# Kernel optimization log

Hardware: AMD Instinct MI355X
Metric: run time of the kernel (lower is better)

Reference implementation:

```python
import jax, jax.numpy as jnp
import numpy as np
import math

B, S, E, H = 4, 2048, 1024, 16
D = E // H  # head_dim = 64


def setup_inputs() -> dict:
    key = jax.random.key(0)
    ks = jax.random.split(key, 12)
    sc = 1.0 / math.sqrt(E)
    inp = {
        "x": jax.random.normal(ks[0], (B, S, E), jnp.float32),
        "mask": jnp.ones((B, S), jnp.int32),
        "text_array": jax.random.normal(ks[1], (B, E), jnp.float32),
        # attention projections, torch Linear convention W:[out,in]
        "Wq": jax.random.normal(ks[2], (E, E), jnp.float32) * sc,
        "bq": jnp.zeros((E,), jnp.float32),
        "Wk": jax.random.normal(ks[3], (E, E), jnp.float32) * sc,
        "bk": jnp.zeros((E,), jnp.float32),
        "Wv": jax.random.normal(ks[4], (E, E), jnp.float32) * sc,
        "bv": jnp.zeros((E,), jnp.float32),
        "Wo": jax.random.normal(ks[5], (E, E), jnp.float32) * sc,
        "bo": jnp.zeros((E,), jnp.float32),
        # TwoLayerMLP head: E -> E//2 -> 1
        "W1": jax.random.normal(ks[6], (E // 2, E), jnp.float32) * sc,
        "b1": jnp.zeros((E // 2,), jnp.float32),
        "W2": jax.random.normal(ks[7], (1, E // 2), jnp.float32) * (1.0 / math.sqrt(E // 2)),
        "b2": jnp.zeros((1,), jnp.float32),
    }
    return inp


def reference(x, mask, text_array, Wq, bq, Wk, bk, Wv, bv, Wo, bo, W1, b1, W2, b2):
    b, s, e = x.shape
    # projections -> [B, S, H, D]
    Q = (x @ Wq.T + bq).reshape(b, s, H, D)
    K = (x @ Wk.T + bk).reshape(b, s, H, D)
    V = (x @ Wv.T + bv).reshape(b, s, H, D)
    # scores [B, H, Sq, Sk]
    scores = jnp.einsum("bqhd,bkhd->bhqk", Q, K) / jnp.sqrt(jnp.asarray(D, x.dtype))
    neg_inf = jnp.asarray(-jnp.inf, scores.dtype)
    scores = jnp.where(mask[:, None, None, :] == 0, neg_inf, scores)
    attn = jax.nn.softmax(scores, axis=-1)  # dropout is identity in eval
    out = jnp.einsum("bhqk,bkhd->bqhd", attn, V).reshape(b, s, e)
    out = out @ Wo.T + bo  # out_proj (out_dropout identity)
    out = out.mean(axis=1)  # [B, E]
    out = out / jnp.linalg.norm(out, axis=-1, keepdims=True)
    out = out - text_array
    h = jax.nn.relu(out @ W1.T + b1)
    score = jnp.tanh(h @ W2.T + b2)  # [B, 1]
    return score
```

## Files before the change

### kernel.cpp

```cpp
#include <hip/hip_runtime.h>

typedef unsigned short ushort_t;
typedef unsigned int uint32;
typedef __attribute__((ext_vector_type(8))) short short8;
typedef __attribute__((ext_vector_type(4))) float f32x4;
typedef __attribute__((ext_vector_type(2))) uint32 uint32x2;

__device__ __forceinline__ ushort_t f2bf(float f) {
  uint32 u = __builtin_bit_cast(uint32, f);
  u = (u + 0x7fffu + ((u >> 16) & 1u)) >> 16;
  return (ushort_t)u;
}

__device__ __forceinline__ float fast_exp2(float x) {
#if __has_builtin(__builtin_amdgcn_exp2f)
  return __builtin_amdgcn_exp2f(x);
#else
  return exp2f(x);
#endif
}

__device__ __forceinline__ uint32 cvt_pk_bf16(float lo, float hi) {
  uint32 r;
  asm("v_cvt_pk_bf16_f32 %0, %1, %2" : "=v"(r) : "v"(lo), "v"(hi));
  return r;
}

__device__ __forceinline__ void gload_lds16(const void* g, void* l) {
  __builtin_amdgcn_global_load_lds(
      (const __attribute__((address_space(1))) void*)g,
      (__attribute__((address_space(3))) void*)l, 16, 0, 0);
}

#define MFMA16(a, b, c) __builtin_amdgcn_mfma_f32_16x16x32_bf16((a), (b), (c), 0, 0, 0)

__global__ void cvt_kernel(const float* __restrict__ src, ushort_t* __restrict__ dst, int n8) {
  int i = blockIdx.x * 256 + threadIdx.x;
  if (i >= n8) return;
  const f32x4* s4 = (const f32x4*)src;
  f32x4 a = s4[2 * i], b = s4[2 * i + 1];
  short8 o;
  o[0] = (short)f2bf(a.x); o[1] = (short)f2bf(a.y); o[2] = (short)f2bf(a.z); o[3] = (short)f2bf(a.w);
  o[4] = (short)f2bf(b.x); o[5] = (short)f2bf(b.y); o[6] = (short)f2bf(b.z); o[7] = (short)f2bf(b.w);
  *(short8*)(dst + 8 * i) = o;
}

__global__ void maskbias_kernel(const int* __restrict__ mask, float* __restrict__ bias, int n) {
  int i = blockIdx.x * 256 + threadIdx.x;
  if (i < n) bias[i] = mask[i] ? 0.f : -30000.f;
}

template <int MODE>
__global__ __launch_bounds__(256, 2) void gemm_bt(const ushort_t* __restrict__ A,
                                                  const ushort_t* __restrict__ Bt,
                                                  const float* __restrict__ bias,
                                                  ushort_t* __restrict__ C, int M, int N, int K,
                                                  float scale) {
  __shared__ ushort_t As[2][128 * 32];
  __shared__ ushort_t Bs[2][128 * 32];
  const int tid = threadIdx.x;
  const int w = tid >> 6, l = tid & 63;
  const int wr = w >> 1, wc = w & 1;
  const int lr = l & 15, g = l >> 4;
  const int bm = blockIdx.y * 128, bn = blockIdx.x * 128;

  const char* gA = (const char*)(A + (size_t)(bm + w * 32 + (l >> 2)) * K + (l & 3) * 8);
  const char* gB = (const char*)(Bt + (size_t)(bn + w * 32 + (l >> 2)) * K + (l & 3) * 8);
  const size_t rowstep = (size_t)16 * K * 2;

  f32x4 acc[4][4] = {};

  auto stage = [&](int buf, int k0) {
    char* dA = (char*)&As[buf][0] + w * 2048;
    char* dB = (char*)&Bs[buf][0] + w * 2048;
    const char* sA = gA + (size_t)k0 * 2;
    const char* sB = gB + (size_t)k0 * 2;
    gload_lds16(sA, dA);
    gload_lds16(sA + rowstep, dA + 1024);
    gload_lds16(sB, dB);
    gload_lds16(sB + rowstep, dB + 1024);
  };

  stage(0, 0);
  __syncthreads();

  const int nk = K >> 5;
  for (int kk = 0; kk < nk; kk++) {
    const int cur = kk & 1;
    if (kk + 1 < nk) stage(cur ^ 1, (kk + 1) << 5);
    short8 af[4], bf[4];
#pragma unroll
    for (int fm = 0; fm < 4; fm++)
      af[fm] = *(const short8*)(&As[cur][(wr * 64 + fm * 16 + lr) * 32 + g * 8]);
#pragma unroll
    for (int fn = 0; fn < 4; fn++)
      bf[fn] = *(const short8*)(&Bs[cur][(wc * 64 + fn * 16 + lr) * 32 + g * 8]);
#pragma unroll
    for (int fm = 0; fm < 4; fm++)
#pragma unroll
      for (int fn = 0; fn < 4; fn++) acc[fm][fn] = MFMA16(af[fm], bf[fn], acc[fm][fn]);
    __syncthreads();
  }

  if (MODE == 0) {
#pragma unroll
    for (int fn = 0; fn < 4; fn++) {
      int col = bn + wc * 64 + fn * 16 + lr;
      float bv = bias[col];
      int h = col >> 6, d = col & 63;
#pragma unroll
      for (int fm = 0; fm < 4; fm++) {
        int rowb = bm + wr * 64 + fm * 16 + g * 4;
#pragma unroll
        for (int j = 0; j < 4; j++) {
          int row = rowb + j;
          int b = row >> 11, s = row & 2047;
          float v = (acc[fm][fn][j] + bv) * scale;
          C[((size_t)(b * 16 + h) * 2048 + s) * 64 + d] = f2bf(v);
        }
      }
    }
  } else {
#pragma unroll
    for (int fm = 0; fm < 4; fm++) {
#pragma unroll
      for (int j = 0; j < 4; j++) {
        int row = bm + wr * 64 + fm * 16 + g * 4 + j;
        float bv = bias[row];
#pragma unroll
        for (int fn = 0; fn < 4; fn++) {
          int col = bn + wc * 64 + fn * 16 + lr;
          C[(size_t)row * N + col] = f2bf(acc[fm][fn][j] + bv);
        }
      }
    }
  }
}

__global__ __launch_bounds__(256, 2) void attn_kernel(const ushort_t* __restrict__ Qb,
                                                      const ushort_t* __restrict__ Kb,
                                                      const ushort_t* __restrict__ Vt,
                                                      const float* __restrict__ mbias,
                                                      float* __restrict__ meanO) {
  __shared__ ushort_t Ks[2][64 * 64];
  __shared__ ushort_t Vs[2][64 * 64];
  __shared__ ushort_t Ps[4][16 * 64];
  __shared__ float bias[2048];

  const int tid = threadIdx.x;
  const int w = tid >> 6, l = tid & 63;
  const int g = l >> 4, qi = l & 15;
  const int xr = qi & 7;
  const int qblk = blockIdx.x, bh = blockIdx.y;
  const int b = bh >> 4, h = bh & 15;
  const int q0 = qblk * 128 + w * 32;

  short8 qf[2][2];
#pragma unroll
  for (int qh = 0; qh < 2; qh++) {
    const ushort_t* qp = Qb + ((size_t)bh * 2048 + q0 + qh * 16 + qi) * 64 + g * 8;
    qf[qh][0] = *(const short8*)qp;
    qf[qh][1] = *(const short8*)(qp + 32);
  }

  {
    const f32x4* bsrc = (const f32x4*)(mbias + b * 2048);
    f32x4* bdst = (f32x4*)bias;
    bdst[tid] = bsrc[tid];
    bdst[tid + 256] = bsrc[tid + 256];
  }

  const int srow = l >> 3;
  const int sch = (l & 7) ^ srow;
  const char* gK = (const char*)Kb + ((size_t)bh * 2048 + w * 8 + srow) * 128 + sch * 16;
  const char* gV = (const char*)Vt +
                   (((size_t)(h * 64 + w * 8 + srow)) * 8192 + (size_t)b * 2048) * 2 + sch * 16;

  auto stage = [&](int buf, int t) {
    const char* sK = gK + (size_t)t * (64 * 128);
    const char* sV = gV + (size_t)t * 128;
    char* dK = (char*)&Ks[buf][0] + w * 1024;
    char* dV = (char*)&Vs[buf][0] + w * 1024;
    gload_lds16(sK, dK);
    gload_lds16(sK + 32 * 128, dK + 4096);
    gload_lds16(sV, dV);
    gload_lds16(sV + (size_t)32 * 16384, dV + 4096);
  };

  float mrun[2] = {-1e30f, -1e30f}, lsum[2] = {0.f, 0.f};
  f32x4 ot[2][4] = {};

  stage(0, 0);
  __syncthreads();

  for (int t = 0; t < 32; t++) {
    const int cur = t & 1;
    if (t < 31) stage(cur ^ 1, t + 1);

    short8 kf[4][2];
#pragma unroll
    for (int fn = 0; fn < 4; fn++) {
      const ushort_t* kr = &Ks[cur][(fn * 16 + qi) * 64];
      kf[fn][0] = *(const short8*)(kr + (g ^ xr) * 8);
      kf[fn][1] = *(const short8*)(kr + ((4 + g) ^ xr) * 8);
    }
    short8 vf[2][4];
#pragma unroll
    for (int tt = 0; tt < 2; tt++)
#pragma unroll
      for (int fd = 0; fd < 4; fd++)
        vf[tt][fd] = *(const short8*)(&Vs[cur][(fd * 16 + qi) * 64] + ((tt * 4 + g) ^ xr) * 8);
    f32x4 bvec[4];
#pragma unroll
    for (int fn = 0; fn < 4; fn++) bvec[fn] = *(const f32x4*)&bias[t * 64 + fn * 16 + g * 4];

    char* Pw = (char*)&Ps[w][0];
#pragma unroll
    for (int qh = 0; qh < 2; qh++) {
      f32x4 sc[4];
#pragma unroll
      for (int fn = 0; fn < 4; fn++) {
        f32x4 z = {};
        z = MFMA16(kf[fn][0], qf[qh][0], z);
        z = MFMA16(kf[fn][1], qf[qh][1], z);
        sc[fn] = z;
      }
      float pmax = -1e30f;
#pragma unroll
      for (int fn = 0; fn < 4; fn++)
#pragma unroll
        for (int j = 0; j < 4; j++) {
          float v = sc[fn][j] + bvec[fn][j];
          sc[fn][j] = v;
          pmax = fmaxf(pmax, v);
        }
      pmax = fmaxf(pmax, __shfl_xor(pmax, 16));
      pmax = fmaxf(pmax, __shfl_xor(pmax, 32));
      if (__any(pmax > mrun[qh] + 8.f)) {
        float mnew = fmaxf(mrun[qh], pmax);
        float r = fast_exp2(mrun[qh] - mnew);
        mrun[qh] = mnew;
        lsum[qh] *= r;
#pragma unroll
        for (int fd = 0; fd < 4; fd++) {
          ot[qh][fd][0] *= r; ot[qh][fd][1] *= r; ot[qh][fd][2] *= r; ot[qh][fd][3] *= r;
        }
      }
      const float m = mrun[qh];
      float psum = 0.f;
      uint32 pk[4][2];
#pragma unroll
      for (int fn = 0; fn < 4; fn++) {
        float p0 = fast_exp2(sc[fn][0] - m);
        float p1 = fast_exp2(sc[fn][1] - m);
        float p2 = fast_exp2(sc[fn][2] - m);
        float p3 = fast_exp2(sc[fn][3] - m);
        psum += (p0 + p1) + (p2 + p3);
        pk[fn][0] = cvt_pk_bf16(p0, p1);
        pk[fn][1] = cvt_pk_bf16(p2, p3);
      }
      psum += __shfl_xor(psum, 16);
      psum += __shfl_xor(psum, 32);
      lsum[qh] += psum;

#pragma unroll
      for (int fn = 0; fn < 4; fn++) {
        uint32x2 pv;
        pv.x = pk[fn][0];
        pv.y = pk[fn][1];
        *(uint32x2*)(Pw + ((qi * 128 + fn * 32 + g * 8) ^ (xr << 4))) = pv;
      }

#pragma unroll
      for (int tt = 0; tt < 2; tt++) {
        short8 bp = *(const short8*)(Pw + ((qi * 128 + tt * 64 + g * 16) ^ (xr << 4)));
#pragma unroll
        for (int fd = 0; fd < 4; fd++) ot[qh][fd] = MFMA16(vf[tt][fd], bp, ot[qh][fd]);
      }
    }
    __syncthreads();
  }

  float rl0 = 1.0f / lsum[0], rl1 = 1.0f / lsum[1];
#pragma unroll
  for (int fd = 0; fd < 4; fd++)
#pragma unroll
    for (int j = 0; j < 4; j++) {
      float v = ot[0][fd][j] * rl0 + ot[1][fd][j] * rl1;
      v += __shfl_xor(v, 1);
      v += __shfl_xor(v, 2);
      v += __shfl_xor(v, 4);
      v += __shfl_xor(v, 8);
      if (qi == 0) atomicAdd(&meanO[b * 1024 + h * 64 + fd * 16 + g * 4 + j], v);
    }
}

__global__ void proj_o(const float* __restrict__ meanO, const float* __restrict__ Wo,
                       const float* __restrict__ bo, float* __restrict__ y) {
  int b = blockIdx.y;
  int t = threadIdx.x;
  int n = blockIdx.x * 64 + (t >> 2);
  int part = t & 3;
  const f32x4* wrow = (const f32x4*)(Wo + (size_t)n * 1024 + part * 256);
  const f32x4* mo = (const f32x4*)(meanO + b * 1024 + part * 256);
  float acc = 0.f;
#pragma unroll 8
  for (int i = 0; i < 64; i++) {
    f32x4 wv = wrow[i], mv = mo[i];
    acc += wv.x * mv.x + wv.y * mv.y + wv.z * mv.z + wv.w * mv.w;
  }
  acc += __shfl_xor(acc, 1);
  acc += __shfl_xor(acc, 2);
  if (part == 0) y[b * 1024 + n] = acc * (1.0f / 2048.0f) + bo[n];
}

__global__ void norm_kernel(const float* __restrict__ y, const float* __restrict__ text,
                            float* __restrict__ u) {
  __shared__ float red[4];
  int b = blockIdx.x, t = threadIdx.x;
  const float* yb = y + b * 1024;
  float ss = 0.f;
  for (int i = t; i < 1024; i += 256) {
    float v = yb[i];
    ss += v * v;
  }
  for (int m = 1; m < 64; m <<= 1) ss += __shfl_xor(ss, m);
  if ((t & 63) == 0) red[t >> 6] = ss;
  __syncthreads();
  float rn = rsqrtf(red[0] + red[1] + red[2] + red[3]);
  for (int i = t; i < 1024; i += 256) u[b * 1024 + i] = yb[i] * rn - text[b * 1024 + i];
}

__global__ void mlp1_kernel(const float* __restrict__ u, const float* __restrict__ W1,
                            const float* __restrict__ b1, float* __restrict__ hb) {
  int b = blockIdx.y;
  int t = threadIdx.x;
  int j = blockIdx.x * 64 + (t >> 2);
  int part = t & 3;
  const f32x4* wr = (const f32x4*)(W1 + (size_t)j * 1024 + part * 256);
  const f32x4* uu = (const f32x4*)(u + b * 1024 + part * 256);
  float a = 0.f;
#pragma unroll 8
  for (int i = 0; i < 64; i++) {
    f32x4 wv = wr[i], uv = uu[i];
    a += wv.x * uv.x + wv.y * uv.y + wv.z * uv.z + wv.w * uv.w;
  }
  a += __shfl_xor(a, 1);
  a += __shfl_xor(a, 2);
  if (part == 0) hb[b * 512 + j] = fmaxf(a + b1[j], 0.f);
}

__global__ void mlp2_kernel(const float* __restrict__ hb, const float* __restrict__ W2,
                            const float* __restrict__ b2, float* __restrict__ out) {
  __shared__ float red[4];
  int b = blockIdx.x, t = threadIdx.x;
  float s2 = 0.f;
  for (int j = t; j < 512; j += 256) s2 += hb[b * 512 + j] * W2[j];
  for (int m = 1; m < 64; m <<= 1) s2 += __shfl_xor(s2, m);
  if ((t & 63) == 0) red[t >> 6] = s2;
  __syncthreads();
  if (t == 0) out[b] = tanhf(red[0] + red[1] + red[2] + red[3] + b2[0]);
}

extern "C" void kernel_launch(void* const* d_in, const int* in_sizes, int n_in, void* d_out,
                              int out_size, void* d_ws, size_t ws_size, hipStream_t stream) {
  (void)in_sizes; (void)n_in; (void)out_size; (void)ws_size;
  const float* x = (const float*)d_in[0];
  const int* mask = (const int*)d_in[1];
  const float* text = (const float*)d_in[2];
  const float* Wq = (const float*)d_in[3];
  const float* bq = (const float*)d_in[4];
  const float* Wk = (const float*)d_in[5];
  const float* bk = (const float*)d_in[6];
  const float* Wv = (const float*)d_in[7];
  const float* bv = (const float*)d_in[8];
  const float* Wo = (const float*)d_in[9];
  const float* bo = (const float*)d_in[10];
  const float* W1 = (const float*)d_in[11];
  const float* b1 = (const float*)d_in[12];
  const float* W2 = (const float*)d_in[13];
  const float* b2 = (const float*)d_in[14];

  char* ws = (char*)d_ws;
  const size_t MB = 1024 * 1024;
  ushort_t* Qb = (ushort_t*)(ws);
  ushort_t* Kb = (ushort_t*)(ws + 16 * MB);
  ushort_t* Vt = (ushort_t*)(ws + 32 * MB);
  ushort_t* xb = (ushort_t*)(ws + 48 * MB);
  ushort_t* wqb = (ushort_t*)(ws + 64 * MB);
  ushort_t* wkb = (ushort_t*)(ws + 66 * MB);
  ushort_t* wvb = (ushort_t*)(ws + 68 * MB);
  float* meanO = (float*)(ws + 70 * MB);
  float* y = (float*)(ws + 70 * MB + 16384);
  float* u = (float*)(ws + 70 * MB + 32768);
  float* hb = (float*)(ws + 70 * MB + 49152);
  float* mbias = (float*)(ws + 70 * MB + 65536);

  cvt_kernel<<<4096, 256, 0, stream>>>(x, xb, 1048576);
  cvt_kernel<<<512, 256, 0, stream>>>(Wq, wqb, 131072);
  cvt_kernel<<<512, 256, 0, stream>>>(Wk, wkb, 131072);
  cvt_kernel<<<512, 256, 0, stream>>>(Wv, wvb, 131072);
  maskbias_kernel<<<32, 256, 0, stream>>>(mask, mbias, 8192);
  hipMemsetAsync(meanO, 0, 4096 * sizeof(float), stream);

  const float qscale = 0.125f * 1.44269504088896f;
  gemm_bt<0><<<dim3(8, 64), 256, 0, stream>>>(xb, wqb, bq, Qb, 8192, 1024, 1024, qscale);
  gemm_bt<0><<<dim3(8, 64), 256, 0, stream>>>(xb, wkb, bk, Kb, 8192, 1024, 1024, 1.0f);
  gemm_bt<1><<<dim3(64, 8), 256, 0, stream>>>(wvb, xb, bv, Vt, 1024, 8192, 1024, 1.0f);

  attn_kernel<<<dim3(16, 64), 256, 0, stream>>>(Qb, Kb, Vt, mbias, meanO);
  proj_o<<<dim3(16, 4), 256, 0, stream>>>(meanO, Wo, bo, y);
  norm_kernel<<<4, 256, 0, stream>>>(y, text, u);
  mlp1_kernel<<<dim3(8, 4), 256, 0, stream>>>(u, W1, b1, hb);
  mlp2_kernel<<<4, 256, 0, stream>>>(hb, W2, b2, (float*)d_out);
}
```

Before: 372.5 us.

## Fuse conversion kernels, merge Q/K GEMMs, fuse MLP tail, read mask bias from global

Merges the four fp32-to-bf16 conversion launches into one, concatenates Wq and Wk so a single GEMM produces both Q and K, and folds norm, MLP1 and MLP2 into one tail kernel. The attention kernel drops its shared-memory mask-bias copy and loads bias vectors straight from global memory each tile. Launch bounds rise to 3 blocks per CU for the GEMMs and 4 for attention. The aim is fewer launches and higher occupancy, at the risk of register spills and of a tail kernel that now runs on only 4 blocks.

```diff
diff --git a/kernel.cpp b/kernel.cpp
--- a/kernel.cpp
+++ b/kernel.cpp
@@ -34,15 +34,29 @@
 
 #define MFMA16(a, b, c) __builtin_amdgcn_mfma_f32_16x16x32_bf16((a), (b), (c), 0, 0, 0)
 
-__global__ void cvt_kernel(const float* __restrict__ src, ushort_t* __restrict__ dst, int n8) {
+__global__ void cvt_all(const float* __restrict__ x, const float* __restrict__ Wq,
+                        const float* __restrict__ Wk, const float* __restrict__ Wv,
+                        ushort_t* __restrict__ xb, ushort_t* __restrict__ wqk,
+                        ushort_t* __restrict__ wv) {
   int i = blockIdx.x * 256 + threadIdx.x;
-  if (i >= n8) return;
+  const float* src;
+  ushort_t* dst;
+  int off;
+  if (i < 1048576) {
+    src = x; dst = xb; off = i;
+  } else if (i < 1048576 + 131072) {
+    src = Wq; dst = wqk; off = i - 1048576;
+  } else if (i < 1048576 + 262144) {
+    src = Wk; dst = wqk + 1048576; off = i - (1048576 + 131072);
+  } else {
+    src = Wv; dst = wv; off = i - (1048576 + 262144);
+  }
   const f32x4* s4 = (const f32x4*)src;
-  f32x4 a = s4[2 * i], b = s4[2 * i + 1];
+  f32x4 a = s4[2 * off], b = s4[2 * off + 1];
   short8 o;
   o[0] = (short)f2bf(a.x); o[1] = (short)f2bf(a.y); o[2] = (short)f2bf(a.z); o[3] = (short)f2bf(a.w);
   o[4] = (short)f2bf(b.x); o[5] = (short)f2bf(b.y); o[6] = (short)f2bf(b.z); o[7] = (short)f2bf(b.w);
-  *(short8*)(dst + 8 * i) = o;
+  *(short8*)(dst + 8 * off) = o;
 }
 
 __global__ void maskbias_kernel(const int* __restrict__ mask, float* __restrict__ bias, int n) {
@@ -50,19 +64,21 @@
   if (i < n) bias[i] = mask[i] ? 0.f : -30000.f;
 }
 
-template <int MODE>
-__global__ __launch_bounds__(256, 2) void gemm_bt(const ushort_t* __restrict__ A,
+__global__ __launch_bounds__(256, 3) void gemm_qk(const ushort_t* __restrict__ A,
                                                   const ushort_t* __restrict__ Bt,
-                                                  const float* __restrict__ bias,
-                                                  ushort_t* __restrict__ C, int M, int N, int K,
-                                                  float scale) {
+                                                  const float* __restrict__ bq,
+                                                  const float* __restrict__ bk,
+                                                  ushort_t* __restrict__ Qb,
+                                                  ushort_t* __restrict__ Kb, float qscale) {
   __shared__ ushort_t As[2][128 * 32];
   __shared__ ushort_t Bs[2][128 * 32];
+  const int K = 1024;
   const int tid = threadIdx.x;
   const int w = tid >> 6, l = tid & 63;
   const int wr = w >> 1, wc = w & 1;
   const int lr = l & 15, g = l >> 4;
   const int bm = blockIdx.y * 128, bn = blockIdx.x * 128;
+  const bool isq = bn < 1024;
 
   const char* gA = (const char*)(A + (size_t)(bm + w * 32 + (l >> 2)) * K + (l & 3) * 8);
   const char* gB = (const char*)(Bt + (size_t)(bn + w * 32 + (l >> 2)) * K + (l & 3) * 8);
@@ -102,42 +118,95 @@
     __syncthreads();
   }
 
-  if (MODE == 0) {
-#pragma unroll
-    for (int fn = 0; fn < 4; fn++) {
-      int col = bn + wc * 64 + fn * 16 + lr;
-      float bv = bias[col];
-      int h = col >> 6, d = col & 63;
-#pragma unroll
-      for (int fm = 0; fm < 4; fm++) {
-        int rowb = bm + wr * 64 + fm * 16 + g * 4;
-#pragma unroll
-        for (int j = 0; j < 4; j++) {
-          int row = rowb + j;
-          int b = row >> 11, s = row & 2047;
-          float v = (acc[fm][fn][j] + bv) * scale;
-          C[((size_t)(b * 16 + h) * 2048 + s) * 64 + d] = f2bf(v);
-        }
-      }
-    }
-  } else {
+  const float* bias = isq ? bq : bk;
+  ushort_t* C = isq ? Qb : Kb;
+  const float scale = isq ? qscale : 1.0f;
+#pragma unroll
+  for (int fn = 0; fn < 4; fn++) {
+    int col = bn + wc * 64 + fn * 16 + lr;
+    int colh = col & 1023;
+    float bv = bias[colh];
+    int h = colh >> 6, d = colh & 63;
 #pragma unroll
     for (int fm = 0; fm < 4; fm++) {
+      int rowb = bm + wr * 64 + fm * 16 + g * 4;
 #pragma unroll
       for (int j = 0; j < 4; j++) {
-        int row = bm + wr * 64 + fm * 16 + g * 4 + j;
-        float bv = bias[row];
-#pragma unroll
-        for (int fn = 0; fn < 4; fn++) {
-          int col = bn + wc * 64 + fn * 16 + lr;
-          C[(size_t)row * N + col] = f2bf(acc[fm][fn][j] + bv);
-        }
-      }
-    }
-  }
-}
-
-__global__ __launch_bounds__(256, 2) void attn_kernel(const ushort_t* __restrict__ Qb,
+        int row = rowb + j;
+        int b = row >> 11, s = row & 2047;
+        float v = (acc[fm][fn][j] + bv) * scale;
+        C[((size_t)(b * 16 + h) * 2048 + s) * 64 + d] = f2bf(v);
+      }
+    }
+  }
+}
+
+__global__ __launch_bounds__(256, 3) void gemm_v(const ushort_t* __restrict__ A,
+                                                 const ushort_t* __restrict__ Bt,
+                                                 const float* __restrict__ bias,
+                                                 ushort_t* __restrict__ C, int M, int N, int K) {
+  __shared__ ushort_t As[2][128 * 32];
+  __shared__ ushort_t Bs[2][128 * 32];
+  const int tid = threadIdx.x;
+  const int w = tid >> 6, l = tid & 63;
+  const int wr = w >> 1, wc = w & 1;
+  const int lr = l & 15, g = l >> 4;
+  const int bm = blockIdx.y * 128, bn = blockIdx.x * 128;
+
+  const char* gA = (const char*)(A + (size_t)(bm + w * 32 + (l >> 2)) * K + (l & 3) * 8);
+  const char* gB = (const char*)(Bt + (size_t)(bn + w * 32 + (l >> 2)) * K + (l & 3) * 8);
+  const size_t rowstep = (size_t)16 * K * 2;
+
+  f32x4 acc[4][4] = {};
+
+  auto stage = [&](int buf, int k0) {
+    char* dA = (char*)&As[buf][0] + w * 2048;
+    char* dB = (char*)&Bs[buf][0] + w * 2048;
+    const char* sA = gA + (size_t)k0 * 2;
+    const char* sB = gB + (size_t)k0 * 2;
+    gload_lds16(sA, dA);
+    gload_lds16(sA + rowstep, dA + 1024);
+    gload_lds16(sB, dB);
+    gload_lds16(sB + rowstep, dB + 1024);
+  };
+
+  stage(0, 0);
+  __syncthreads();
+
+  const int nk = K >> 5;
+  for (int kk = 0; kk < nk; kk++) {
+    const int cur = kk & 1;
+    if (kk + 1 < nk) stage(cur ^ 1, (kk + 1) << 5);
+    short8 af[4], bf[4];
+#pragma unroll
+    for (int fm = 0; fm < 4; fm++)
+      af[fm] = *(const short8*)(&As[cur][(wr * 64 + fm * 16 + lr) * 32 + g * 8]);
+#pragma unroll
+    for (int fn = 0; fn < 4; fn++)
+      bf[fn] = *(const short8*)(&Bs[cur][(wc * 64 + fn * 16 + lr) * 32 + g * 8]);
+#pragma unroll
+    for (int fm = 0; fm < 4; fm++)
+#pragma unroll
+      for (int fn = 0; fn < 4; fn++) acc[fm][fn] = MFMA16(af[fm], bf[fn], acc[fm][fn]);
+    __syncthreads();
+  }
+
+#pragma unroll
+  for (int fm = 0; fm < 4; fm++) {
+#pragma unroll
+    for (int j = 0; j < 4; j++) {
+      int row = bm + wr * 64 + fm * 16 + g * 4 + j;
+      float bv = bias[row];
+#pragma unroll
+      for (int fn = 0; fn < 4; fn++) {
+        int col = bn + wc * 64 + fn * 16 + lr;
+        C[(size_t)row * N + col] = f2bf(acc[fm][fn][j] + bv);
+      }
+    }
+  }
+}
+
+__global__ __launch_bounds__(256, 4) void attn_kernel(const ushort_t* __restrict__ Qb,
                                                       const ushort_t* __restrict__ Kb,
                                                       const ushort_t* __restrict__ Vt,
                                                       const float* __restrict__ mbias,
@@ -145,7 +214,6 @@
   __shared__ ushort_t Ks[2][64 * 64];
   __shared__ ushort_t Vs[2][64 * 64];
   __shared__ ushort_t Ps[4][16 * 64];
-  __shared__ float bias[2048];
 
   const int tid = threadIdx.x;
   const int w = tid >> 6, l = tid & 63;
@@ -163,18 +231,12 @@
     qf[qh][1] = *(const short8*)(qp + 32);
   }
 
-  {
-    const f32x4* bsrc = (const f32x4*)(mbias + b * 2048);
-    f32x4* bdst = (f32x4*)bias;
-    bdst[tid] = bsrc[tid];
-    bdst[tid + 256] = bsrc[tid + 256];
-  }
-
   const int srow = l >> 3;
   const int sch = (l & 7) ^ srow;
   const char* gK = (const char*)Kb + ((size_t)bh * 2048 + w * 8 + srow) * 128 + sch * 16;
   const char* gV = (const char*)Vt +
                    (((size_t)(h * 64 + w * 8 + srow)) * 8192 + (size_t)b * 2048) * 2 + sch * 16;
+  const float* bbase = mbias + b * 2048 + g * 4;
 
   auto stage = [&](int buf, int t) {
     const char* sK = gK + (size_t)t * (64 * 128);
@@ -195,6 +257,10 @@
 
   for (int t = 0; t < 32; t++) {
     const int cur = t & 1;
+    f32x4 bvec[4];
+#pragma unroll
+    for (int fn = 0; fn < 4; fn++) bvec[fn] = *(const f32x4*)(bbase + t * 64 + fn * 16);
+
     if (t < 31) stage(cur ^ 1, t + 1);
 
     short8 kf[4][2];
@@ -210,9 +276,6 @@
 #pragma unroll
       for (int fd = 0; fd < 4; fd++)
         vf[tt][fd] = *(const short8*)(&Vs[cur][(fd * 16 + qi) * 64] + ((tt * 4 + g) ^ xr) * 8);
-    f32x4 bvec[4];
-#pragma unroll
-    for (int fn = 0; fn < 4; fn++) bvec[fn] = *(const f32x4*)&bias[t * 64 + fn * 16 + g * 4];
 
     char* Pw = (char*)&Ps[w][0];
 #pragma unroll
@@ -314,11 +377,16 @@
   if (part == 0) y[b * 1024 + n] = acc * (1.0f / 2048.0f) + bo[n];
 }
 
-__global__ void norm_kernel(const float* __restrict__ y, const float* __restrict__ text,
-                            float* __restrict__ u) {
-  __shared__ float red[4];
+__global__ void tail_kernel(const float* __restrict__ y, const float* __restrict__ text,
+                            const float* __restrict__ W1, const float* __restrict__ b1,
+                            const float* __restrict__ W2, const float* __restrict__ b2,
+                            float* __restrict__ out) {
+  __shared__ float u[1024];
+  __shared__ float hbuf[512];
+  __shared__ float red[8];
   int b = blockIdx.x, t = threadIdx.x;
   const float* yb = y + b * 1024;
+
   float ss = 0.f;
   for (int i = t; i < 1024; i += 256) {
     float v = yb[i];
@@ -328,34 +396,28 @@
   if ((t & 63) == 0) red[t >> 6] = ss;
   __syncthreads();
   float rn = rsqrtf(red[0] + red[1] + red[2] + red[3]);
-  for (int i = t; i < 1024; i += 256) u[b * 1024 + i] = yb[i] * rn - text[b * 1024 + i];
-}
-
-__global__ void mlp1_kernel(const float* __restrict__ u, const float* __restrict__ W1,
-                            const float* __restrict__ b1, float* __restrict__ hb) {
-  int b = blockIdx.y;
-  int t = threadIdx.x;
-  int j = blockIdx.x * 64 + (t >> 2);
-  int part = t & 3;
-  const f32x4* wr = (const f32x4*)(W1 + (size_t)j * 1024 + part * 256);
-  const f32x4* uu = (const f32x4*)(u + b * 1024 + part * 256);
-  float a = 0.f;
+  for (int i = t; i < 1024; i += 256) u[i] = yb[i] * rn - text[b * 1024 + i];
+  __syncthreads();
+
+  int grp = t >> 2, part = t & 3;
+  for (int p = 0; p < 8; p++) {
+    int j = p * 64 + grp;
+    const f32x4* wr = (const f32x4*)(W1 + (size_t)j * 1024 + part * 256);
+    const f32x4* uu = (const f32x4*)(u + part * 256);
+    float a = 0.f;
 #pragma unroll 8
-  for (int i = 0; i < 64; i++) {
-    f32x4 wv = wr[i], uv = uu[i];
-    a += wv.x * uv.x + wv.y * uv.y + wv.z * uv.z + wv.w * uv.w;
-  }
-  a += __shfl_xor(a, 1);
-  a += __shfl_xor(a, 2);
-  if (part == 0) hb[b * 512 + j] = fmaxf(a + b1[j], 0.f);
-}
-
-__global__ void mlp2_kernel(const float* __restrict__ hb, const float* __restrict__ W2,
-                            const float* __restrict__ b2, float* __restrict__ out) {
-  __shared__ float red[4];
-  int b = blockIdx.x, t = threadIdx.x;
+    for (int i = 0; i < 64; i++) {
+      f32x4 wv = wr[i], uv = uu[i];
+      a += wv.x * uv.x + wv.y * uv.y + wv.z * uv.z + wv.w * uv.w;
+    }
+    a += __shfl_xor(a, 1);
+    a += __shfl_xor(a, 2);
+    if (part == 0) hbuf[j] = fmaxf(a + b1[j], 0.f);
+  }
+  __syncthreads();
+
   float s2 = 0.f;
-  for (int j = t; j < 512; j += 256) s2 += hb[b * 512 + j] * W2[j];
+  for (int j = t; j < 512; j += 256) s2 += hbuf[j] * W2[j];
   for (int m = 1; m < 64; m <<= 1) s2 += __shfl_xor(s2, m);
   if ((t & 63) == 0) red[t >> 6] = s2;
   __syncthreads();
@@ -387,30 +449,21 @@
   ushort_t* Kb = (ushort_t*)(ws + 16 * MB);
   ushort_t* Vt = (ushort_t*)(ws + 32 * MB);
   ushort_t* xb = (ushort_t*)(ws + 48 * MB);
-  ushort_t* wqb = (ushort_t*)(ws + 64 * MB);
-  ushort_t* wkb = (ushort_t*)(ws + 66 * MB);
+  ushort_t* wqk = (ushort_t*)(ws + 64 * MB);
   ushort_t* wvb = (ushort_t*)(ws + 68 * MB);
   float* meanO = (float*)(ws + 70 * MB);
   float* y = (float*)(ws + 70 * MB + 16384);
-  float* u = (float*)(ws + 70 * MB + 32768);
-  float* hb = (float*)(ws + 70 * MB + 49152);
   float* mbias = (float*)(ws + 70 * MB + 65536);
 
-  cvt_kernel<<<4096, 256, 0, stream>>>(x, xb, 1048576);
-  cvt_kernel<<<512, 256, 0, stream>>>(Wq, wqb, 131072);
-  cvt_kernel<<<512, 256, 0, stream>>>(Wk, wkb, 131072);
-  cvt_kernel<<<512, 256, 0, stream>>>(Wv, wvb, 131072);
+  cvt_all<<<5632, 256, 0, stream>>>(x, Wq, Wk, Wv, xb, wqk, wvb);
   maskbias_kernel<<<32, 256, 0, stream>>>(mask, mbias, 8192);
   hipMemsetAsync(meanO, 0, 4096 * sizeof(float), stream);
 
   const float qscale = 0.125f * 1.44269504088896f;
-  gemm_bt<0><<<dim3(8, 64), 256, 0, stream>>>(xb, wqb, bq, Qb, 8192, 1024, 1024, qscale);
-  gemm_bt<0><<<dim3(8, 64), 256, 0, stream>>>(xb, wkb, bk, Kb, 8192, 1024, 1024, 1.0f);
-  gemm_bt<1><<<dim3(64, 8), 256, 0, stream>>>(wvb, xb, bv, Vt, 1024, 8192, 1024, 1.0f);
+  gemm_qk<<<dim3(16, 64), 256, 0, stream>>>(xb, wqk, bq, bk, Qb, Kb, qscale);
+  gemm_v<<<dim3(64, 8), 256, 0, stream>>>(wvb, xb, bv, Vt, 1024, 8192, 1024);
 
   attn_kernel<<<dim3(16, 64), 256, 0, stream>>>(Qb, Kb, Vt, mbias, meanO);
   proj_o<<<dim3(16, 4), 256, 0, stream>>>(meanO, Wo, bo, y);
-  norm_kernel<<<4, 256, 0, stream>>>(y, text, u);
-  mlp1_kernel<<<dim3(8, 4), 256, 0, stream>>>(u, W1, b1, hb);
-  mlp2_kernel<<<4, 256, 0, stream>>>(hb, W2, b2, (float*)d_out);
-}
+  tail_kernel<<<4, 256, 0, stream>>>(y, text, W1, b1, W2, b2, (float*)d_out);
+}
```

After: 889.7 us. 2.39x slower.
